# Performance work log

Measured on AMD Instinct MI355X. Metric: run time of the kernel, lower is better.

## Reference

```python
import jax, jax.numpy as jnp
import numpy as np

N_NODES = 50000
N_EDGES = 20000
EDGE_SIZE = 32
IN_CH = 256
OUT_CH = 256


def setup_inputs() -> dict:
    key = jax.random.key(0)
    k1, k2, k3 = jax.random.split(key, 3)
    x = jax.random.normal(k1, (N_NODES, IN_CH), dtype=jnp.float32)
    hyperedges = jax.random.randint(k2, (N_EDGES, EDGE_SIZE), 0, N_NODES)
    weight = jax.random.normal(k3, (IN_CH, OUT_CH), dtype=jnp.float32)
    return {"x": x, "hyperedges": hyperedges, "weight": weight}


def reference(x, hyperedges, weight):
    # Gather node features per hyperedge and reduce ('sum' aggregation):
    # [E, K, C] -> [E, C]
    edge_sum = x[hyperedges].sum(axis=1)
    # Scatter-add each hyperedge's summed feature back to every member node.
    agg = jnp.zeros_like(x).at[hyperedges].add(edge_sum[:, None, :])
    # Dense projection + ReLU.
    return jax.nn.relu(agg @ weight)
```

## Files before the change

kernel.cpp:

```cpp
#include <hip/hip_runtime.h>
#include <hip/hip_bf16.h>
#include <hip/hip_fp16.h>

#define N_NODES 50000
#define N_EDGES 20000
#define EDGE_K  32
#define CH      256
#define N_INC   (N_EDGES * EDGE_K)
#define ELL_CAP 64
#define NSLICE  8
#define SCH     32
#define ZROW    N_EDGES

typedef __attribute__((ext_vector_type(4))) float f32x4;
typedef __attribute__((ext_vector_type(8))) _Float16 f16x8;

static __device__ __forceinline__ __half2 u2h2(unsigned int u) {
    __half2 h; __builtin_memcpy(&h, &u, 4); return h;
}
static __device__ __forceinline__ unsigned int h22u(__half2 h) {
    unsigned int u; __builtin_memcpy(&u, &h, 4); return u;
}
static __device__ __forceinline__ unsigned int pk2h(float a, float b) {
    return h22u(__halves2half2(__float2half_rn(a), __float2half_rn(b)));
}

#define CONV_BLOCKS (N_NODES * CH / 8 / 256)
#define ELLI_BLOCKS (N_NODES * ELL_CAP / 2 / 256)
__global__ void prep_kernel(const float* __restrict__ x, unsigned short* __restrict__ xb,
                            const float* __restrict__ w, unsigned short* __restrict__ wt,
                            unsigned int* __restrict__ ellu, unsigned short* __restrict__ yb) {
    int b = blockIdx.x;
    if (b < CONV_BLOCKS) {
        int i = b * 256 + threadIdx.x;
        int n = i >> 5, sub = i & 31;
        int g = sub >> 2, cp = (sub & 3) * 8;
        const float* src = x + (size_t)n * CH + sub * 8;
        f32x4 v0 = *reinterpret_cast<const f32x4*>(src);
        f32x4 v1 = *reinterpret_cast<const f32x4*>(src + 4);
        uint4 u;
        u.x = pk2h(v0.x, v0.y);
        u.y = pk2h(v0.z, v0.w);
        u.z = pk2h(v1.x, v1.y);
        u.w = pk2h(v1.z, v1.w);
        *reinterpret_cast<uint4*>(xb + ((size_t)g * N_NODES + n) * SCH + cp) = u;
    } else if (b < CONV_BLOCKS + ELLI_BLOCKS) {
        int i = (b - CONV_BLOCKS) * 256 + threadIdx.x;
        ellu[i] = 0x4E204E20u;
    } else if (b < CONV_BLOCKS + ELLI_BLOCKS + CH) {
        int n = b - CONV_BLOCKS - ELLI_BLOCKS;
        int k = threadIdx.x;
        __half h = __float2half_rn(w[k * CH + n]);
        wt[n * CH + k] = *reinterpret_cast<unsigned short*>(&h);
    } else {
        int g = threadIdx.x >> 5, c = threadIdx.x & 31;
        yb[((size_t)g * (N_EDGES + 1) + ZROW) * SCH + c] = 0;
    }
}

#define FILL_GROUPS   8
#define NODES_PER_GRP (N_NODES / FILL_GROUPS)
#define FILL_WIN      2560
#define FILL_BLOCKS   ((N_INC / FILL_WIN) * FILL_GROUPS)
#define GATHER_BLOCKS ((N_EDGES / 16) * NSLICE)
__global__ __launch_bounds__(256, 4) void gather_fill_kernel(
        const unsigned short* __restrict__ xb, const int* __restrict__ he,
        unsigned short* __restrict__ es, int* __restrict__ deg,
        unsigned short* __restrict__ ell) {
    int b = blockIdx.x;
    if (b < FILL_BLOCKS) {
        int g  = b & 7;
        int wn = b >> 3;
        int lo = g * NODES_PER_GRP, hi = lo + NODES_PER_GRP;
        int base = wn * FILL_WIN;
#pragma unroll
        for (int it = 0; it < FILL_WIN / 256; ++it) {
            int i = base + it * 256 + threadIdx.x;
            int node = he[i];
            if (node >= lo && node < hi) {
                int slot = atomicAdd(&deg[node], 1);
                if (slot < ELL_CAP)
                    ell[(size_t)node * ELL_CAP + slot] = (unsigned short)(i >> 5);
            }
        }
        return;
    }
    int gb  = b - FILL_BLOCKS;
    int g   = gb & 7;
    int grp = gb >> 3;
    int w = threadIdx.x >> 6, lane = threadIdx.x & 63;
    int ebase = grp * 16 + w * 4;
    const int* hp = he + (size_t)ebase * EDGE_K;
    int s = lane & 15;
    int ep = lane >> 4, k = (lane >> 2) & 3, q = lane & 3;
    int mA = hp[ep * 32 + s];
    int mB = hp[ep * 32 + 16 + s];
    const unsigned short* xg = xb + (size_t)g * N_NODES * SCH;
    int hb = lane & 48;
    int e0 = __shfl(mA, hb + ((0 + k) & 15), 64);
    int e1 = __shfl(mA, hb + ((4 + k) & 15), 64);
    int e2 = __shfl(mA, hb + ((8 + k) & 15), 64);
    int e3 = __shfl(mA, hb + ((12 + k) & 15), 64);
    int e4 = __shfl(mB, hb + ((0 + k) & 15), 64);
    int e5 = __shfl(mB, hb + ((4 + k) & 15), 64);
    int e6 = __shfl(mB, hb + ((8 + k) & 15), 64);
    int e7 = __shfl(mB, hb + ((12 + k) & 15), 64);
    uint4 d0 = *reinterpret_cast<const uint4*>(xg + (size_t)e0 * SCH + q * 8);
    uint4 d1 = *reinterpret_cast<const uint4*>(xg + (size_t)e1 * SCH + q * 8);
    uint4 d2 = *reinterpret_cast<const uint4*>(xg + (size_t)e2 * SCH + q * 8);
    uint4 d3 = *reinterpret_cast<const uint4*>(xg + (size_t)e3 * SCH + q * 8);
    uint4 d4 = *reinterpret_cast<const uint4*>(xg + (size_t)e4 * SCH + q * 8);
    uint4 d5 = *reinterpret_cast<const uint4*>(xg + (size_t)e5 * SCH + q * 8);
    uint4 d6 = *reinterpret_cast<const uint4*>(xg + (size_t)e6 * SCH + q * 8);
    uint4 d7 = *reinterpret_cast<const uint4*>(xg + (size_t)e7 * SCH + q * 8);
    __half2 a0 = u2h2(0u), a1 = u2h2(0u), a2 = u2h2(0u), a3 = u2h2(0u);
    a0 = __hadd2(a0, u2h2(d0.x)); a1 = __hadd2(a1, u2h2(d0.y));
    a2 = __hadd2(a2, u2h2(d0.z)); a3 = __hadd2(a3, u2h2(d0.w));
    a0 = __hadd2(a0, u2h2(d1.x)); a1 = __hadd2(a1, u2h2(d1.y));
    a2 = __hadd2(a2, u2h2(d1.z)); a3 = __hadd2(a3, u2h2(d1.w));
    a0 = __hadd2(a0, u2h2(d2.x)); a1 = __hadd2(a1, u2h2(d2.y));
    a2 = __hadd2(a2, u2h2(d2.z)); a3 = __hadd2(a3, u2h2(d2.w));
    a0 = __hadd2(a0, u2h2(d3.x)); a1 = __hadd2(a1, u2h2(d3.y));
    a2 = __hadd2(a2, u2h2(d3.z)); a3 = __hadd2(a3, u2h2(d3.w));
    a0 = __hadd2(a0, u2h2(d4.x)); a1 = __hadd2(a1, u2h2(d4.y));
    a2 = __hadd2(a2, u2h2(d4.z)); a3 = __hadd2(a3, u2h2(d4.w));
    a0 = __hadd2(a0, u2h2(d5.x)); a1 = __hadd2(a1, u2h2(d5.y));
    a2 = __hadd2(a2, u2h2(d5.z)); a3 = __hadd2(a3, u2h2(d5.w));
    a0 = __hadd2(a0, u2h2(d6.x)); a1 = __hadd2(a1, u2h2(d6.y));
    a2 = __hadd2(a2, u2h2(d6.z)); a3 = __hadd2(a3, u2h2(d6.w));
    a0 = __hadd2(a0, u2h2(d7.x)); a1 = __hadd2(a1, u2h2(d7.y));
    a2 = __hadd2(a2, u2h2(d7.z)); a3 = __hadd2(a3, u2h2(d7.w));
    a0 = __hadd2(a0, u2h2(__shfl_xor(h22u(a0), 4, 64)));
    a1 = __hadd2(a1, u2h2(__shfl_xor(h22u(a1), 4, 64)));
    a2 = __hadd2(a2, u2h2(__shfl_xor(h22u(a2), 4, 64)));
    a3 = __hadd2(a3, u2h2(__shfl_xor(h22u(a3), 4, 64)));
    a0 = __hadd2(a0, u2h2(__shfl_xor(h22u(a0), 8, 64)));
    a1 = __hadd2(a1, u2h2(__shfl_xor(h22u(a1), 8, 64)));
    a2 = __hadd2(a2, u2h2(__shfl_xor(h22u(a2), 8, 64)));
    a3 = __hadd2(a3, u2h2(__shfl_xor(h22u(a3), 8, 64)));
    if ((lane & 12) == 0) {
        uint4 u;
        u.x = h22u(a0); u.y = h22u(a1); u.z = h22u(a2); u.w = h22u(a3);
        *reinterpret_cast<uint4*>(es + (size_t)(ebase + ep) * CH + g * SCH + q * 8) = u;
    }
}

__global__ __launch_bounds__(256) void gemm_kernel(const unsigned short* __restrict__ es,
                                                   const unsigned short* __restrict__ wt,
                                                   unsigned short* __restrict__ yb) {
    int wid  = threadIdx.x >> 6;
    int lane = threadIdx.x & 63;
    int m0   = blockIdx.x * 64 + wid * 16;
    if (m0 >= N_EDGES) return;
    int lr = lane & 15;
    int lg = lane >> 4;

    f32x4 acc[16] = {};
    const unsigned short* arow = es + (size_t)(m0 + lr) * CH + lg * 8;
#pragma unroll
    for (int kk = 0; kk < CH; kk += 32) {
        f16x8 a = *reinterpret_cast<const f16x8*>(arow + kk);
#pragma unroll
        for (int nt = 0; nt < 16; ++nt) {
            f16x8 bb = *reinterpret_cast<const f16x8*>(
                wt + (size_t)(nt * 16 + lr) * CH + kk + lg * 8);
            acc[nt] = __builtin_amdgcn_mfma_f32_16x16x32_f16(a, bb, acc[nt], 0, 0, 0);
        }
    }
#pragma unroll
    for (int nt = 0; nt < 16; ++nt) {
#pragma unroll
        for (int r = 0; r < 4; ++r) {
            int row = m0 + lg * 4 + r;
            __half h = __float2half_rn(acc[nt][r]);
            yb[((size_t)(nt >> 1) * (N_EDGES + 1) + row) * SCH + (nt & 1) * 16 + lr] =
                *reinterpret_cast<unsigned short*>(&h);
        }
    }
}

#define AP_NPB    16
#define AP_BLOCKS ((N_NODES / AP_NPB) * NSLICE)
__global__ __launch_bounds__(256, 4) void apply_kernel(
        const unsigned short* __restrict__ yb, const int* __restrict__ deg,
        const unsigned short* __restrict__ ell, float* __restrict__ out) {
    int b = blockIdx.x;
    int g = b & 7;
    int w = threadIdx.x >> 6, lane = threadIdx.x & 63;
    int np = lane >> 4, s = lane & 15, k = (lane >> 2) & 3, q = lane & 3;
    int node = (b >> 3) * AP_NPB + w * 4 + np;
    int d = deg[node];
    const unsigned short* er = ell + (size_t)node * ELL_CAP;
    int m0 = er[s], m1 = er[16 + s];
    int dmax = d;
    dmax = max(dmax, __shfl_xor(dmax, 16, 64));
    dmax = max(dmax, __shfl_xor(dmax, 32, 64));
    const unsigned short* yg = yb + (size_t)g * (N_EDGES + 1) * SCH;
    int hb = lane & 48;
    int e0 = __shfl(m0, hb + 0 + k, 64);
    int e1 = __shfl(m0, hb + 4 + k, 64);
    int e2 = __shfl(m0, hb + 8 + k, 64);
    int e3 = __shfl(m0, hb + 12 + k, 64);
    uint4 d0 = *reinterpret_cast<const uint4*>(yg + (size_t)e0 * SCH + q * 8);
    uint4 d1 = *reinterpret_cast<const uint4*>(yg + (size_t)e1 * SCH + q * 8);
    uint4 d2 = *reinterpret_cast<const uint4*>(yg + (size_t)e2 * SCH + q * 8);
    uint4 d3 = *reinterpret_cast<const uint4*>(yg + (size_t)e3 * SCH + q * 8);
    __half2 a0 = __hadd2(u2h2(d0.x), u2h2(d1.x));
    __half2 a1 = __hadd2(u2h2(d0.y), u2h2(d1.y));
    __half2 a2 = __hadd2(u2h2(d0.z), u2h2(d1.z));
    __half2 a3 = __hadd2(u2h2(d0.w), u2h2(d1.w));
    a0 = __hadd2(a0, u2h2(d2.x)); a1 = __hadd2(a1, u2h2(d2.y));
    a2 = __hadd2(a2, u2h2(d2.z)); a3 = __hadd2(a3, u2h2(d2.w));
    a0 = __hadd2(a0, u2h2(d3.x)); a1 = __hadd2(a1, u2h2(d3.y));
    a2 = __hadd2(a2, u2h2(d3.z)); a3 = __hadd2(a3, u2h2(d3.w));
    if (dmax > 16) {
        int f0 = __shfl(m1, hb + 0 + k, 64);
        int f1 = __shfl(m1, hb + 4 + k, 64);
        int f2 = __shfl(m1, hb + 8 + k, 64);
        int f3 = __shfl(m1, hb + 12 + k, 64);
        uint4 c0 = *reinterpret_cast<const uint4*>(yg + (size_t)f0 * SCH + q * 8);
        uint4 c1 = *reinterpret_cast<const uint4*>(yg + (size_t)f1 * SCH + q * 8);
        uint4 c2 = *reinterpret_cast<const uint4*>(yg + (size_t)f2 * SCH + q * 8);
        uint4 c3 = *reinterpret_cast<const uint4*>(yg + (size_t)f3 * SCH + q * 8);
        a0 = __hadd2(a0, u2h2(c0.x)); a1 = __hadd2(a1, u2h2(c0.y));
        a2 = __hadd2(a2, u2h2(c0.z)); a3 = __hadd2(a3, u2h2(c0.w));
        a0 = __hadd2(a0, u2h2(c1.x)); a1 = __hadd2(a1, u2h2(c1.y));
        a2 = __hadd2(a2, u2h2(c1.z)); a3 = __hadd2(a3, u2h2(c1.w));
        a0 = __hadd2(a0, u2h2(c2.x)); a1 = __hadd2(a1, u2h2(c2.y));
        a2 = __hadd2(a2, u2h2(c2.z)); a3 = __hadd2(a3, u2h2(c2.w));
        a0 = __hadd2(a0, u2h2(c3.x)); a1 = __hadd2(a1, u2h2(c3.y));
        a2 = __hadd2(a2, u2h2(c3.z)); a3 = __hadd2(a3, u2h2(c3.w));
    }
    if (dmax > 32) {
        int m2 = er[32 + s], m3 = er[48 + s];
#pragma unroll
        for (int rq = 0; rq < 2; ++rq) {
            int m = rq ? m3 : m2;
            int f0 = __shfl(m, hb + 0 + k, 64);
            int f1 = __shfl(m, hb + 4 + k, 64);
            int f2 = __shfl(m, hb + 8 + k, 64);
            int f3 = __shfl(m, hb + 12 + k, 64);
            uint4 c0 = *reinterpret_cast<const uint4*>(yg + (size_t)f0 * SCH + q * 8);
            uint4 c1 = *reinterpret_cast<const uint4*>(yg + (size_t)f1 * SCH + q * 8);
            uint4 c2 = *reinterpret_cast<const uint4*>(yg + (size_t)f2 * SCH + q * 8);
            uint4 c3 = *reinterpret_cast<const uint4*>(yg + (size_t)f3 * SCH + q * 8);
            a0 = __hadd2(a0, u2h2(c0.x)); a1 = __hadd2(a1, u2h2(c0.y));
            a2 = __hadd2(a2, u2h2(c0.z)); a3 = __hadd2(a3, u2h2(c0.w));
            a0 = __hadd2(a0, u2h2(c1.x)); a1 = __hadd2(a1, u2h2(c1.y));
            a2 = __hadd2(a2, u2h2(c1.z)); a3 = __hadd2(a3, u2h2(c1.w));
            a0 = __hadd2(a0, u2h2(c2.x)); a1 = __hadd2(a1, u2h2(c2.y));
            a2 = __hadd2(a2, u2h2(c2.z)); a3 = __hadd2(a3, u2h2(c2.w));
            a0 = __hadd2(a0, u2h2(c3.x)); a1 = __hadd2(a1, u2h2(c3.y));
            a2 = __hadd2(a2, u2h2(c3.z)); a3 = __hadd2(a3, u2h2(c3.w));
        }
    }
    a0 = __hadd2(a0, u2h2(__shfl_xor(h22u(a0), 4, 64)));
    a1 = __hadd2(a1, u2h2(__shfl_xor(h22u(a1), 4, 64)));
    a2 = __hadd2(a2, u2h2(__shfl_xor(h22u(a2), 4, 64)));
    a3 = __hadd2(a3, u2h2(__shfl_xor(h22u(a3), 4, 64)));
    a0 = __hadd2(a0, u2h2(__shfl_xor(h22u(a0), 8, 64)));
    a1 = __hadd2(a1, u2h2(__shfl_xor(h22u(a1), 8, 64)));
    a2 = __hadd2(a2, u2h2(__shfl_xor(h22u(a2), 8, 64)));
    a3 = __hadd2(a3, u2h2(__shfl_xor(h22u(a3), 8, 64)));
    if ((lane & 12) == 0) {
        float2 f0 = __half22float2(a0);
        float2 f1 = __half22float2(a1);
        float2 f2 = __half22float2(a2);
        float2 f3 = __half22float2(a3);
        f32x4 r0, r1;
        r0.x = fmaxf(f0.x, 0.f); r0.y = fmaxf(f0.y, 0.f);
        r0.z = fmaxf(f1.x, 0.f); r0.w = fmaxf(f1.y, 0.f);
        r1.x = fmaxf(f2.x, 0.f); r1.y = fmaxf(f2.y, 0.f);
        r1.z = fmaxf(f3.x, 0.f); r1.w = fmaxf(f3.y, 0.f);
        float* dst = out + (size_t)node * CH + g * SCH + q * 8;
        *reinterpret_cast<f32x4*>(dst)     = r0;
        *reinterpret_cast<f32x4*>(dst + 4) = r1;
    }
}

extern "C" void kernel_launch(void* const* d_in, const int* in_sizes, int n_in,
                              void* d_out, int out_size, void* d_ws, size_t ws_size,
                              hipStream_t stream) {
    const float* x  = (const float*)d_in[0];
    const int*   he = (const int*)d_in[1];
    const float* w  = (const float*)d_in[2];
    float* out = (float*)d_out;

    char* ws = (char*)d_ws;
    unsigned short* wt  = (unsigned short*)ws;
    unsigned short* es  = (unsigned short*)(ws + 131072);
    unsigned short* yb  = (unsigned short*)(ws + 10371072);
    int* deg = (int*)(ws + 20611584);
    unsigned short* ell = (unsigned short*)(ws + 20811584);

    unsigned short* xb = (unsigned short*)d_out;

    hipMemsetAsync(deg, 0, (size_t)N_NODES * 4, stream);

    prep_kernel<<<CONV_BLOCKS + ELLI_BLOCKS + CH + 1, 256, 0, stream>>>(
        x, xb, w, wt, (unsigned int*)ell, yb);

    gather_fill_kernel<<<FILL_BLOCKS + GATHER_BLOCKS, 256, 0, stream>>>(xb, he, es, deg, ell);

    {
        int blocks = (N_EDGES + 63) / 64;
        gemm_kernel<<<blocks, 256, 0, stream>>>(es, wt, yb);
    }

    apply_kernel<<<AP_BLOCKS, 256, 0, stream>>>(yb, deg, ell, out);
}
```

Measured before the change: 144.4 us.

## Move ELL fill into prep kernel and initialize ELL via memset

Moves the hyperedge-to-node ELL fill (atomic degree counting) out of the gather kernel and interleaves those blocks with the fp16 conversion blocks of the prep kernel. The conversion is bandwidth-bound and the fill is atomic-latency-bound, so running them together is meant to overlap the two. ELL sentinel initialization now uses a byte memset (0x4E4E), so the zero-row index and the yb row stride change to match. It adds a memset launch, and correctness now depends on the memset finishing before the fill, which stream ordering guarantees.

```diff
diff --git a/kernel.cpp b/kernel.cpp
--- a/kernel.cpp
+++ b/kernel.cpp
@@ -10,7 +10,8 @@
 #define ELL_CAP 64
 #define NSLICE  8
 #define SCH     32
-#define ZROW    N_EDGES
+#define ZROW    0x4E4E
+#define EROWS   20047
 
 typedef __attribute__((ext_vector_type(4))) float f32x4;
 typedef __attribute__((ext_vector_type(8))) _Float16 f16x8;
@@ -25,14 +26,38 @@
     return h22u(__halves2half2(__float2half_rn(a), __float2half_rn(b)));
 }
 
-#define CONV_BLOCKS (N_NODES * CH / 8 / 256)
-#define ELLI_BLOCKS (N_NODES * ELL_CAP / 2 / 256)
+#define FILL_GROUPS   8
+#define NODES_PER_GRP (N_NODES / FILL_GROUPS)
+#define FILL_WIN      2560
+#define FILL_BODIES   ((N_INC / FILL_WIN) * FILL_GROUPS)
+#define CONV_BLOCKS   (N_NODES * CH / 8 / 256)
+#define PREP_GRID     8507
 __global__ void prep_kernel(const float* __restrict__ x, unsigned short* __restrict__ xb,
                             const float* __restrict__ w, unsigned short* __restrict__ wt,
-                            unsigned int* __restrict__ ellu, unsigned short* __restrict__ yb) {
+                            const int* __restrict__ he, int* __restrict__ deg,
+                            unsigned short* __restrict__ ell, unsigned short* __restrict__ yb) {
     int b = blockIdx.x;
-    if (b < CONV_BLOCKS) {
-        int i = b * 256 + threadIdx.x;
+    if (b < 8000 && (b & 3) == 3) {
+        int fb = b >> 2;
+        int g  = fb & 7;
+        int wn = fb >> 3;
+        int lo = g * NODES_PER_GRP, hi = lo + NODES_PER_GRP;
+        int base = wn * FILL_WIN;
+#pragma unroll
+        for (int it = 0; it < FILL_WIN / 256; ++it) {
+            int i = base + it * 256 + threadIdx.x;
+            int node = he[i];
+            if (node >= lo && node < hi) {
+                int slot = atomicAdd(&deg[node], 1);
+                if (slot < ELL_CAP)
+                    ell[(size_t)node * ELL_CAP + slot] = (unsigned short)(i >> 5);
+            }
+        }
+        return;
+    }
+    int cb = (b < 8000) ? (b - (b >> 2)) : (b - 2000);
+    if (cb < CONV_BLOCKS) {
+        int i = cb * 256 + threadIdx.x;
         int n = i >> 5, sub = i & 31;
         int g = sub >> 2, cp = (sub & 3) * 8;
         const float* src = x + (size_t)n * CH + sub * 8;
@@ -44,48 +69,22 @@
         u.z = pk2h(v1.x, v1.y);
         u.w = pk2h(v1.z, v1.w);
         *reinterpret_cast<uint4*>(xb + ((size_t)g * N_NODES + n) * SCH + cp) = u;
-    } else if (b < CONV_BLOCKS + ELLI_BLOCKS) {
-        int i = (b - CONV_BLOCKS) * 256 + threadIdx.x;
-        ellu[i] = 0x4E204E20u;
-    } else if (b < CONV_BLOCKS + ELLI_BLOCKS + CH) {
-        int n = b - CONV_BLOCKS - ELLI_BLOCKS;
+    } else if (cb < CONV_BLOCKS + CH) {
+        int n = cb - CONV_BLOCKS;
         int k = threadIdx.x;
         __half h = __float2half_rn(w[k * CH + n]);
         wt[n * CH + k] = *reinterpret_cast<unsigned short*>(&h);
-    } else {
+    } else if (cb == CONV_BLOCKS + CH) {
         int g = threadIdx.x >> 5, c = threadIdx.x & 31;
-        yb[((size_t)g * (N_EDGES + 1) + ZROW) * SCH + c] = 0;
-    }
-}
-
-#define FILL_GROUPS   8
-#define NODES_PER_GRP (N_NODES / FILL_GROUPS)
-#define FILL_WIN      2560
-#define FILL_BLOCKS   ((N_INC / FILL_WIN) * FILL_GROUPS)
+        yb[((size_t)g * EROWS + ZROW) * SCH + c] = 0;
+    }
+}
+
 #define GATHER_BLOCKS ((N_EDGES / 16) * NSLICE)
-__global__ __launch_bounds__(256, 4) void gather_fill_kernel(
+__global__ __launch_bounds__(256, 4) void gather_kernel(
         const unsigned short* __restrict__ xb, const int* __restrict__ he,
-        unsigned short* __restrict__ es, int* __restrict__ deg,
-        unsigned short* __restrict__ ell) {
-    int b = blockIdx.x;
-    if (b < FILL_BLOCKS) {
-        int g  = b & 7;
-        int wn = b >> 3;
-        int lo = g * NODES_PER_GRP, hi = lo + NODES_PER_GRP;
-        int base = wn * FILL_WIN;
-#pragma unroll
-        for (int it = 0; it < FILL_WIN / 256; ++it) {
-            int i = base + it * 256 + threadIdx.x;
-            int node = he[i];
-            if (node >= lo && node < hi) {
-                int slot = atomicAdd(&deg[node], 1);
-                if (slot < ELL_CAP)
-                    ell[(size_t)node * ELL_CAP + slot] = (unsigned short)(i >> 5);
-            }
-        }
-        return;
-    }
-    int gb  = b - FILL_BLOCKS;
+        unsigned short* __restrict__ es) {
+    int gb  = blockIdx.x;
     int g   = gb & 7;
     int grp = gb >> 3;
     int w = threadIdx.x >> 6, lane = threadIdx.x & 63;
@@ -173,7 +172,7 @@
         for (int r = 0; r < 4; ++r) {
             int row = m0 + lg * 4 + r;
             __half h = __float2half_rn(acc[nt][r]);
-            yb[((size_t)(nt >> 1) * (N_EDGES + 1) + row) * SCH + (nt & 1) * 16 + lr] =
+            yb[((size_t)(nt >> 1) * EROWS + row) * SCH + (nt & 1) * 16 + lr] =
                 *reinterpret_cast<unsigned short*>(&h);
         }
     }
@@ -195,7 +194,7 @@
     int dmax = d;
     dmax = max(dmax, __shfl_xor(dmax, 16, 64));
     dmax = max(dmax, __shfl_xor(dmax, 32, 64));
-    const unsigned short* yg = yb + (size_t)g * (N_EDGES + 1) * SCH;
+    const unsigned short* yg = yb + (size_t)g * EROWS * SCH;
     int hb = lane & 48;
     int e0 = __shfl(m0, hb + 0 + k, 64);
     int e1 = __shfl(m0, hb + 4 + k, 64);
@@ -290,17 +289,17 @@
     unsigned short* wt  = (unsigned short*)ws;
     unsigned short* es  = (unsigned short*)(ws + 131072);
     unsigned short* yb  = (unsigned short*)(ws + 10371072);
-    int* deg = (int*)(ws + 20611584);
-    unsigned short* ell = (unsigned short*)(ws + 20811584);
+    int* deg = (int*)(ws + 20635136);
+    unsigned short* ell = (unsigned short*)(ws + 20835136);
 
     unsigned short* xb = (unsigned short*)d_out;
 
     hipMemsetAsync(deg, 0, (size_t)N_NODES * 4, stream);
-
-    prep_kernel<<<CONV_BLOCKS + ELLI_BLOCKS + CH + 1, 256, 0, stream>>>(
-        x, xb, w, wt, (unsigned int*)ell, yb);
-
-    gather_fill_kernel<<<FILL_BLOCKS + GATHER_BLOCKS, 256, 0, stream>>>(xb, he, es, deg, ell);
+    hipMemsetAsync(ell, 0x4E, (size_t)N_NODES * ELL_CAP * 2, stream);
+
+    prep_kernel<<<PREP_GRID, 256, 0, stream>>>(x, xb, w, wt, he, deg, ell, yb);
+
+    gather_kernel<<<GATHER_BLOCKS, 256, 0, stream>>>(xb, he, es);
 
     {
         int blocks = (N_EDGES + 63) / 64;
```

Result: slower. 152.9 us (+5.9%).
